# Kernel optimization log

Hardware: AMD Instinct MI355X
Metric: run time of the kernel (lower is better)

The kernel has to match this reference:

```python
import jax, jax.numpy as jnp
import numpy as np

B, D, H, U, K, IV = 4096, 512, 512, 8, 5, 400
NH, CK, CV = 4, 32, 100  # comm heads, comm key/query size, comm value size

@jax.custom_vjp
def blocked_grad(x, mask):
    return x

def _bg_fwd(x, mask):
    return x, mask

def _bg_bwd(mask, g):
    return (g * mask, jnp.zeros_like(mask))

blocked_grad.defvjp(_bg_fwd, _bg_bwd)

def _ln(x, g, b, eps=1e-5):
    m = jnp.mean(x, -1, keepdims=True)
    v = jnp.var(x, -1, keepdims=True)
    return (x - m) / jnp.sqrt(v + eps) * g + b

def setup_inputs():
    key = jax.random.key(0)
    ks = jax.random.split(key, 16)
    def u(k, shape, fan_in):
        lim = 1.0 / np.sqrt(fan_in)
        return jax.random.uniform(k, shape, jnp.float32, -lim, lim)
    return dict(
        x=jax.random.normal(ks[0], (B, 1, D), jnp.float32),
        hs=jax.random.normal(ks[1], (B, U, H), jnp.float32),
        h_masks=jnp.ones((B, 1), jnp.float32),
        key_w=u(ks[2], (D, 64), D), key_b=jnp.zeros((64,), jnp.float32),
        value_w=u(ks[3], (D, IV), D), value_b=jnp.zeros((IV,), jnp.float32),
        query_w=u(ks[4], (U, H, 64), H),
        qc_w=u(ks[5], (U, H, NH * CK), H),
        kc_w=u(ks[6], (U, H, NH * CK), H),
        vc_w=u(ks[7], (U, H, NH * CV), H),
        out_w=u(ks[8], (U, NH * CV, H), NH * CV),
        ln_g=jnp.ones((H,), jnp.float32), ln_b=jnp.zeros((H,), jnp.float32),
        W_ih=u(ks[9], (U, 3 * H, IV), IV), b_ih=jnp.zeros((U, 3 * H), jnp.float32),
        W_hh=u(ks[10], (U, 3 * H, H), H), b_hh=jnp.zeros((U, 3 * H), jnp.float32),
        rnn_ln_g=jnp.ones((U, H), jnp.float32), rnn_ln_b=jnp.zeros((U, H), jnp.float32),
    )

def _forward(x, hs, h_masks, key_w, key_b, value_w, value_b, query_w, qc_w, kc_w,
             vc_w, out_w, ln_g, ln_b, W_ih, b_ih, W_hh, b_hh, rnn_ln_g, rnn_ln_b):
    b = x.shape[0]
    # ---- input attention with top-k unit selection ----
    x2 = jnp.concatenate([x, jnp.zeros_like(x)], axis=1)            # [B,2,D] (null input appended)
    k_l = x2 @ key_w + key_b                                        # [B,2,64]
    v_l = x2 @ value_w + value_b                                    # [B,2,IV]
    q_l = jnp.einsum('buh,uhk->buk', hs, query_w)                   # [B,U,64] grouped linear
    scores = jnp.einsum('buk,btk->but', q_l, k_l) / np.sqrt(64.0)   # [B,U,2]
    _, idx = jax.lax.top_k(scores[:, :, 0], K)                      # top-k over not-null scores
    mask = jnp.zeros((b, U), x.dtype).at[jnp.arange(b)[:, None], idx].set(1.0)
    probs = jax.nn.softmax(scores, axis=-1)                         # dropout is identity at eval
    inp = jnp.einsum('but,btv->buv', probs, v_l) * mask[:, :, None]  # [B,U,IV]
    h_old = hs
    # ---- per-unit GRU (MAPPO RNNLayer: mask hidden, GRU step, LayerNorm on output) ----
    hm = hs * h_masks.reshape(b, 1, 1)
    gi = jnp.einsum('buv,ugv->bug', inp, W_ih) + b_ih               # [B,U,3H]
    gh = jnp.einsum('buh,ugh->bug', hm, W_hh) + b_hh                # [B,U,3H]
    i_r, i_z, i_n = jnp.split(gi, 3, axis=-1)
    h_r, h_z, h_n = jnp.split(gh, 3, axis=-1)
    r = jax.nn.sigmoid(i_r + h_r)
    z = jax.nn.sigmoid(i_z + h_z)
    n = jnp.tanh(i_n + r * h_n)
    h_new = (1.0 - z) * n + z * hm                                  # [B,U,H]
    y = _ln(h_new, rnn_ln_g, rnn_ln_b)
    x_final = y.reshape(b, 1, U * H)
    mask3 = mask[:, :, None]
    hb = blocked_grad(h_new, mask3)
    # ---- communication attention over units (4 heads) ----
    qc = jnp.einsum('buh,uhk->buk', hb, qc_w).reshape(b, U, NH, CK).transpose(0, 2, 1, 3)
    kc = jnp.einsum('buh,uhk->buk', hb, kc_w).reshape(b, U, NH, CK).transpose(0, 2, 1, 3)
    vc = jnp.einsum('buh,uhk->buk', hb, vc_w).reshape(b, U, NH, CV).transpose(0, 2, 1, 3)
    att = jnp.einsum('bnuk,bnvk->bnuv', qc, kc) / np.sqrt(float(CK))
    ap = jax.nn.softmax(att, axis=-1) * mask[:, None, :, None]      # mask query rows
    ctx = jnp.einsum('bnuv,bnvc->bnuc', ap, vc).transpose(0, 2, 1, 3).reshape(b, U, NH * CV)
    ctx = jnp.einsum('buv,uvh->buh', ctx, out_w)                    # grouped output projection
    h_comm = _ln(ctx + hb, ln_g, ln_b)
    hs_out = mask3 * h_comm + (1.0 - mask3) * h_old
    return x_final, hs_out

def reference(x, hs, h_masks, key_w, key_b, value_w, value_b, query_w, qc_w, kc_w,
              vc_w, out_w, ln_g, ln_b, W_ih, b_ih, W_hh, b_hh, rnn_ln_g, rnn_ln_b):
    return _forward(x, hs, h_masks, key_w, key_b, value_w, value_b, query_w, qc_w,
                    kc_w, vc_w, out_w, ln_g, ln_b, W_ih, b_ih, W_hh, b_hh,
                    rnn_ln_g, rnn_ln_b)
```

## Files before the change

### kernel.cpp

```cpp
#include <hip/hip_runtime.h>

typedef __attribute__((ext_vector_type(4))) float f32x4;
typedef __attribute__((ext_vector_type(8))) short bf16x8;
typedef unsigned short u16;

#define DEVINL static __device__ __forceinline__

DEVINL float b2f(u16 u) { union { unsigned int i; float f; } x; x.i = ((unsigned int)u) << 16; return x.f; }
DEVINL u16 f2bf(float f) {
  union { float f; unsigned int i; } x; x.f = f;
  unsigned int r = x.i + 0x7fffu + ((x.i >> 16) & 1u);
  return (u16)(r >> 16);
}
DEVINL float ldin(const void* p, long i, int f) {
  return f ? ((const float*)p)[i] : b2f(((const u16*)p)[i]);
}
DEVINL void ld4bf(const u16* p, float* o) {
  ushort4 v = *(const ushort4*)p;
  o[0] = b2f(v.x); o[1] = b2f(v.y); o[2] = b2f(v.z); o[3] = b2f(v.w);
}
DEVINL void st4out(void* out, size_t idx, const float* v, int f) {
  if (f) {
    float4 t; t.x = v[0]; t.y = v[1]; t.z = v[2]; t.w = v[3];
    *(float4*)((float*)out + idx) = t;
  } else {
    ushort4 t; t.x = f2bf(v[0]); t.y = f2bf(v[1]); t.z = f2bf(v[2]); t.w = f2bf(v[3]);
    *(ushort4*)((u16*)out + idx) = t;
  }
}
DEVINL void cv8(const void* s, long i, int f, u16* d) {
  if (f) {
    const float4 a = *(const float4*)((const float*)s + i);
    const float4 b = *(const float4*)((const float*)s + i + 4);
    ushort4 lo, hi;
    lo.x = f2bf(a.x); lo.y = f2bf(a.y); lo.z = f2bf(a.z); lo.w = f2bf(a.w);
    hi.x = f2bf(b.x); hi.y = f2bf(b.y); hi.z = f2bf(b.z); hi.w = f2bf(b.w);
    *(ushort4*)d = lo; *(ushort4*)(d + 4) = hi;
  } else {
    const ushort4 a = *(const ushort4*)((const u16*)s + i);
    const ushort4 b = *(const ushort4*)((const u16*)s + i + 4);
    *(ushort4*)d = a; *(ushort4*)(d + 4) = b;
  }
}

static constexpr size_t OFF_FLAG = 0;
static constexpr size_t OFF_WIH  = 1024;
static constexpr size_t OFF_QVW  = 11011072;
static constexpr size_t OFF_OUTW = 23593984;
static constexpr size_t OFF_VALW = 27264000;
static constexpr size_t OFF_WHH  = 27788288;
static constexpr size_t OFF_VBP  = 40371200;
static constexpr size_t OFF_BIH  = 40372224;
static constexpr size_t OFF_BHH  = 40396800;
static constexpr size_t OFF_RNG  = 40421376;
static constexpr size_t OFF_RNB  = 40429568;
static constexpr size_t OFF_LNG  = 40437760;
static constexpr size_t OFF_LNB  = 40438784;
static constexpr size_t OFF_HMF  = 40439808;
static constexpr size_t OFF_XB   = 40456192;
static constexpr size_t OFF_HSB  = 44650496;
static constexpr size_t OFF_KL   = 78204928;
static constexpr size_t OFF_VL   = 79253504;
static constexpr size_t OFF_QL   = 87642112;
static constexpr size_t OFF_MASK = 96030720;
static constexpr size_t OFF_HB   = 96161792;
static constexpr size_t OFF_R    = 129716224;

__global__ __launch_bounds__(256) void detect_kernel(const u16* __restrict__ hs_u, int* __restrict__ flag) {
  __shared__ int cnt;
  if (threadIdx.x == 0) cnt = 0;
  __syncthreads();
  int ok = 0;
  for (int i = threadIdx.x; i < 1024; i += 256) {
    const float v = fabsf(b2f(hs_u[2 * i]));
    if (v > 9.094947e-13f && v < 1.0995116e12f) ok++;
  }
  atomicAdd(&cnt, ok);
  __syncthreads();
  if (threadIdx.x == 0) flag[0] = (cnt >= 921) ? 0 : 1;
}

__global__ __launch_bounds__(256) void flatconv_kernel(
    const void* __restrict__ W_ih, const void* __restrict__ W_hh, const void* __restrict__ x,
    const void* __restrict__ hs, const void* __restrict__ value_b, const void* __restrict__ b_ih,
    const void* __restrict__ b_hh, const void* __restrict__ rnn_g, const void* __restrict__ rnn_b,
    const void* __restrict__ ln_g, const void* __restrict__ ln_b, const void* __restrict__ h_masks,
    const int* __restrict__ flagp,
    u16* __restrict__ WIH, u16* __restrict__ WHH, u16* __restrict__ XB, u16* __restrict__ HSB,
    u16* __restrict__ VBP, u16* __restrict__ BIH, u16* __restrict__ BHH,
    u16* __restrict__ RNG, u16* __restrict__ RNB, u16* __restrict__ LNG, u16* __restrict__ LNB,
    float* __restrict__ HMF)
{
  const int f = flagp[0];
  long t = (long)blockIdx.x * 256 + threadIdx.x;
  if (t < 688128L) {
    const long r = t / 56; const int k = (int)(t - r * 56) * 8;
    u16* d = WIH + r * 448 + k;
    if (k < 400) cv8(W_ih, r * 400 + k, f, d);
    else { ushort4 z{0,0,0,0}; *(ushort4*)d = z; *(ushort4*)(d + 4) = z; }
    return;
  }
  t -= 688128L;
  if (t < 786432L) { cv8(W_hh, t * 8, f, WHH + t * 8); return; }
  t -= 786432L;
  if (t < 262144L) { cv8(x, t * 8, f, XB + t * 8); return; }
  t -= 262144L;
  if (t < 2097152L) { cv8(hs, t * 8, f, HSB + t * 8); return; }
  t -= 2097152L;
  if (t < 512L) { VBP[t] = (t < 400) ? f2bf(ldin(value_b, t, f)) : (u16)0; return; }
  t -= 512L;
  if (t < 12288L) { BIH[t] = f2bf(ldin(b_ih, t, f)); return; }
  t -= 12288L;
  if (t < 12288L) { BHH[t] = f2bf(ldin(b_hh, t, f)); return; }
  t -= 12288L;
  if (t < 4096L) { RNG[t] = f2bf(ldin(rnn_g, t, f)); return; }
  t -= 4096L;
  if (t < 4096L) { RNB[t] = f2bf(ldin(rnn_b, t, f)); return; }
  t -= 4096L;
  if (t < 512L) { LNG[t] = f2bf(ldin(ln_g, t, f)); return; }
  t -= 512L;
  if (t < 512L) { LNB[t] = f2bf(ldin(ln_b, t, f)); return; }
  t -= 512L;
  if (t < 4096L) { HMF[t] = ldin(h_masks, t, f); return; }
}

__global__ __launch_bounds__(256) void transpose_kernel(
    const void* __restrict__ src, const int* __restrict__ flagp, u16* __restrict__ dst,
    int K, int N, int Kp, long srcZ, long dstZ)
{
  const int f = flagp[0];
  __shared__ float t[64][65];
  const int k0 = blockIdx.x * 64, n0 = blockIdx.y * 64, z = blockIdx.z;
  const int tid = threadIdx.x;
  const int lk = tid >> 4;
  const int ln4 = (tid & 15) * 4;
#pragma unroll
  for (int p = 0; p < 4; ++p) {
    const int k = k0 + lk + p * 16;
    float v[4] = {0.f, 0.f, 0.f, 0.f};
    if (k < K) {
      const long base = srcZ * z + (long)k * N + n0 + ln4;
#pragma unroll
      for (int j = 0; j < 4; ++j)
        if (n0 + ln4 + j < N) v[j] = ldin(src, base + j, f);
    }
    t[lk + p * 16][ln4 + 0] = v[0]; t[lk + p * 16][ln4 + 1] = v[1];
    t[lk + p * 16][ln4 + 2] = v[2]; t[lk + p * 16][ln4 + 3] = v[3];
  }
  __syncthreads();
#pragma unroll
  for (int p = 0; p < 4; ++p) {
    const int n = n0 + lk + p * 16;
    ushort4 o;
    o.x = f2bf(t[ln4 + 0][lk + p * 16]);
    o.y = f2bf(t[ln4 + 1][lk + p * 16]);
    o.z = f2bf(t[ln4 + 2][lk + p * 16]);
    o.w = f2bf(t[ln4 + 3][lk + p * 16]);
    *(ushort4*)&dst[dstZ * z + (long)n * Kp + k0 + ln4] = o;
  }
}

template<int OUT_BF16, int HAS_BIAS>
__global__ __launch_bounds__(256) void gemm_bt_kernel(
    const u16* __restrict__ A, const u16* __restrict__ W, void* __restrict__ Cp,
    const u16* __restrict__ bias, int KP, int ldaE, long Az, long Wz, long Cz, int Bz, int ldc)
{
  __shared__ u16 lA[128 * 64];
  __shared__ u16 lB[128 * 64];
  const int tid = threadIdx.x;
  const int m0 = blockIdx.x * 128, n0 = blockIdx.y * 128, z = blockIdx.z;
  const u16* Au = A + (size_t)z * Az;
  const u16* Wu = W + (size_t)z * Wz;

  const int l = tid & 63, w = tid >> 6;
  const int WM = (w >> 1) * 64, WN = (w & 1) * 64;
  const int lr = l & 15, kg = l >> 4;

  f32x4 acc[4][4];
#pragma unroll
  for (int i = 0; i < 4; ++i)
#pragma unroll
    for (int j = 0; j < 4; ++j) acc[i][j] = (f32x4){0.f, 0.f, 0.f, 0.f};

  const int rowA = tid >> 3;
  const int cb = (tid & 7) * 16;
  const size_t rowBytesA = (size_t)ldaE * 2;
  const size_t rowBytesW = (size_t)KP * 2;

  for (int k0 = 0; k0 < KP; k0 += 64) {
    __syncthreads();
    const char* gA = (const char*)Au + (size_t)(m0 + rowA) * rowBytesA + (size_t)k0 * 2 + cb;
    const char* gB = (const char*)Wu + (size_t)(n0 + rowA) * rowBytesW + (size_t)k0 * 2 + cb;
    char* sA = (char*)lA + (w << 10);
    char* sB = (char*)lB + (w << 10);
#pragma unroll
    for (int c = 0; c < 4; ++c) {
      __builtin_amdgcn_global_load_lds(
          (const __attribute__((address_space(1))) void*)(gA + (size_t)c * 32 * rowBytesA),
          (__attribute__((address_space(3))) void*)(sA + c * 4096), 16, 0, 0);
      __builtin_amdgcn_global_load_lds(
          (const __attribute__((address_space(1))) void*)(gB + (size_t)c * 32 * rowBytesW),
          (__attribute__((address_space(3))) void*)(sB + c * 4096), 16, 0, 0);
    }
    __syncthreads();
#pragma unroll
    for (int kk = 0; kk < 64; kk += 32) {
      bf16x8 af[4], bw[4];
#pragma unroll
      for (int i = 0; i < 4; ++i)
        af[i] = *(const bf16x8*)&lA[(WM + i * 16 + lr) * 64 + kk + kg * 8];
#pragma unroll
      for (int j = 0; j < 4; ++j)
        bw[j] = *(const bf16x8*)&lB[(WN + j * 16 + lr) * 64 + kk + kg * 8];
#pragma unroll
      for (int i = 0; i < 4; ++i)
#pragma unroll
        for (int j = 0; j < 4; ++j)
          acc[i][j] = __builtin_amdgcn_mfma_f32_16x16x32_bf16(af[i], bw[j], acc[i][j], 0, 0, 0);
    }
  }
  float* Cf = (float*)Cp;
  u16* Cb = (u16*)Cp;
#pragma unroll
  for (int i = 0; i < 4; ++i) {
#pragma unroll
    for (int j = 0; j < 4; ++j) {
      const int gc = n0 + WN + j * 16 + lr;
      float bv = 0.f;
      if (HAS_BIAS) bv = b2f(bias[(size_t)z * Bz + gc]);
#pragma unroll
      for (int t = 0; t < 4; ++t) {
        const int gr = m0 + WM + i * 16 + kg * 4 + t;
        const float v = acc[i][j][t] + bv;
        const size_t idx = (size_t)z * Cz + (size_t)gr * ldc + gc;
        if (OUT_BF16) Cb[idx] = f2bf(v); else Cf[idx] = v;
      }
    }
  }
}

__global__ __launch_bounds__(256) void gemm_f32bf_kernel(
    const void* __restrict__ A, const void* __restrict__ W, float* __restrict__ C,
    const void* __restrict__ bias, const int* __restrict__ flagp,
    int K, int lda, int ldw, int ldc, long Az, long Wz, long Cz)
{
  const int f32 = flagp[0];
  __shared__ float sA[16][65];
  __shared__ float sW[16][64];
  const int tid = threadIdx.x;
  const int m0 = blockIdx.x * 64, n0 = blockIdx.y * 64, z = blockIdx.z;
  const int tx = tid & 15, ty = tid >> 4;
  const int ar = tid >> 2, ak = (tid & 3) * 4;
  const int wk = tid >> 4, wc = (tid & 15) * 4;
  const size_t abase = (size_t)z * Az, wbase = (size_t)z * Wz;
  float acc[4][4] = {};
  for (int k0 = 0; k0 < K; k0 += 16) {
    __syncthreads();
    float a0, a1, a2, a3, w0, w1, w2, w3;
    const size_t ai = abase + (size_t)(m0 + ar) * lda + k0 + ak;
    const size_t wi = wbase + (size_t)(k0 + wk) * ldw + n0 + wc;
    if (f32) {
      const float4 av = *(const float4*)((const float*)A + ai);
      const float4 wv = *(const float4*)((const float*)W + wi);
      a0 = av.x; a1 = av.y; a2 = av.z; a3 = av.w;
      w0 = wv.x; w1 = wv.y; w2 = wv.z; w3 = wv.w;
    } else {
      const ushort4 av = *(const ushort4*)((const u16*)A + ai);
      const ushort4 wv = *(const ushort4*)((const u16*)W + wi);
      a0 = b2f(av.x); a1 = b2f(av.y); a2 = b2f(av.z); a3 = b2f(av.w);
      w0 = b2f(wv.x); w1 = b2f(wv.y); w2 = b2f(wv.z); w3 = b2f(wv.w);
    }
    sA[ak + 0][ar] = a0; sA[ak + 1][ar] = a1; sA[ak + 2][ar] = a2; sA[ak + 3][ar] = a3;
    sW[wk][wc] = w0; sW[wk][wc + 1] = w1; sW[wk][wc + 2] = w2; sW[wk][wc + 3] = w3;
    __syncthreads();
#pragma unroll
    for (int kk = 0; kk < 16; ++kk) {
      const float a0c = sA[kk][ty * 4 + 0], a1c = sA[kk][ty * 4 + 1];
      const float a2c = sA[kk][ty * 4 + 2], a3c = sA[kk][ty * 4 + 3];
      const float4 bv = *(const float4*)&sW[kk][tx * 4];
      acc[0][0] += a0c * bv.x; acc[0][1] += a0c * bv.y; acc[0][2] += a0c * bv.z; acc[0][3] += a0c * bv.w;
      acc[1][0] += a1c * bv.x; acc[1][1] += a1c * bv.y; acc[1][2] += a1c * bv.z; acc[1][3] += a1c * bv.w;
      acc[2][0] += a2c * bv.x; acc[2][1] += a2c * bv.y; acc[2][2] += a2c * bv.z; acc[2][3] += a2c * bv.w;
      acc[3][0] += a3c * bv.x; acc[3][1] += a3c * bv.y; acc[3][2] += a3c * bv.z; acc[3][3] += a3c * bv.w;
    }
  }
#pragma unroll
  for (int i = 0; i < 4; ++i)
#pragma unroll
    for (int j = 0; j < 4; ++j) {
      const int n = n0 + tx * 4 + j;
      float v = acc[i][j];
      if (bias) v += ldin(bias, n, f32);
      C[(size_t)z * Cz + (size_t)(m0 + ty * 4 + i) * ldc + n] = v;
    }
}

__global__ __launch_bounds__(256) void select_kernel(
    const float* __restrict__ q_l, const float* __restrict__ k_l,
    const void* __restrict__ key_b, const void* __restrict__ value_b,
    const float* __restrict__ v_l, const int* __restrict__ flagp,
    float* __restrict__ mask_out, u16* __restrict__ inp)
{
  const int b = blockIdx.x, tid = threadIdx.x;
  const int f32 = flagp[0];
  __shared__ float s_sc[16], s_pm[8], s_pm1[8];
  __shared__ float s_v[400], s_vb[400];
  const int task = tid >> 4, l16 = tid & 15, uu = task & 7;
  const float* qv = q_l + (size_t)b * 512 + uu * 64;
  float p = 0.f;
  if (task < 8) {
    const float* kv = k_l + (size_t)b * 64;
    for (int k = l16; k < 64; k += 16) p += qv[k] * kv[k];
  } else {
    for (int k = l16; k < 64; k += 16) p += qv[k] * ldin(key_b, k, f32);
  }
  p += __shfl_xor(p, 8, 16); p += __shfl_xor(p, 4, 16);
  p += __shfl_xor(p, 2, 16); p += __shfl_xor(p, 1, 16);
  if (l16 == 0) s_sc[task] = p * 0.125f;
  for (int i = tid; i < 400; i += 256) { s_v[i] = v_l[(size_t)b * 512 + i]; s_vb[i] = ldin(value_b, i, f32); }
  __syncthreads();
  if (tid < 8) {
    const float s0 = s_sc[tid];
    int rank = 0;
    for (int u2 = 0; u2 < 8; ++u2) {
      const float o = s_sc[u2];
      rank += (o > s0) || (o == s0 && u2 < tid);
    }
    const float m = (rank < 5) ? 1.f : 0.f;
    mask_out[(size_t)b * 8 + tid] = m;
    const float s1 = s_sc[8 + tid];
    const float mx = fmaxf(s0, s1);
    const float e0 = expf(s0 - mx), e1 = expf(s1 - mx);
    const float p0 = e0 / (e0 + e1);
    s_pm[tid] = m * p0; s_pm1[tid] = m * (1.f - p0);
  }
  __syncthreads();
#pragma unroll
  for (int u = 0; u < 8; ++u) {
    const float pm = s_pm[u], pm1 = s_pm1[u];
    for (int i = tid; i < 448; i += 256) {
      const float v = (i < 400) ? (pm * s_v[i] + pm1 * s_vb[i]) : 0.f;
      inp[((size_t)u * 4096 + b) * 448 + i] = f2bf(v);
    }
  }
}

__device__ __forceinline__ void block_reduce_2(float& a, float& b) {
#pragma unroll
  for (int o = 32; o; o >>= 1) { a += __shfl_down(a, o, 64); b += __shfl_down(b, o, 64); }
  __shared__ float red[4];
  const int tid = threadIdx.x;
  if ((tid & 63) == 0) { red[(tid >> 6) * 2] = a; red[(tid >> 6) * 2 + 1] = b; }
  __syncthreads();
  a = red[0] + red[2]; b = red[1] + red[3];
}

__global__ __launch_bounds__(128) void gates_kernel(
    const u16* __restrict__ gi, const u16* __restrict__ gh,
    const u16* __restrict__ hsb, const float* __restrict__ hmf,
    const u16* __restrict__ bhh, const u16* __restrict__ rng, const u16* __restrict__ rnb,
    const int* __restrict__ flagp, int bbase, void* __restrict__ out0, u16* __restrict__ hb)
{
  const int f = flagp[0];
  const int u = blockIdx.y, bl = blockIdx.x;
  const int b = bbase + bl;
  const int h0 = threadIdx.x * 4;
  const size_t rowg = ((size_t)u * gridDim.x + bl) * 1536;
  const size_t rowhs = ((size_t)b * 8 + u) * 512;
  const size_t rowhb = ((size_t)u * 4096 + b) * 512;
  float ir[4], iz[4], inn[4], hr[4], hz[4], hnn[4], hsv[4], br[4], bz[4], bn[4];
  ld4bf(gi + rowg + h0, ir);
  ld4bf(gi + rowg + 512 + h0, iz);
  ld4bf(gi + rowg + 1024 + h0, inn);
  ld4bf(gh + rowg + h0, hr);
  ld4bf(gh + rowg + 512 + h0, hz);
  ld4bf(gh + rowg + 1024 + h0, hnn);
  ld4bf(hsb + rowhs + h0, hsv);
  ld4bf(bhh + u * 1536 + h0, br);
  ld4bf(bhh + u * 1536 + 512 + h0, bz);
  ld4bf(bhh + u * 1536 + 1024 + h0, bn);
  const float hmask = hmf[b];
  float hn[4]; float sum = 0.f, sq = 0.f;
#pragma unroll
  for (int j = 0; j < 4; ++j) {
    const float hrf = hmask * hr[j] + br[j];
    const float hzf = hmask * hz[j] + bz[j];
    const float hnf = hmask * hnn[j] + bn[j];
    const float r = 1.f / (1.f + expf(-(ir[j] + hrf)));
    const float zz = 1.f / (1.f + expf(-(iz[j] + hzf)));
    const float n = tanhf(inn[j] + r * hnf);
    const float hmv = hsv[j] * hmask;
    const float h = (1.f - zz) * n + zz * hmv;
    hn[j] = h; sum += h; sq += h * h;
  }
  block_reduce_2(sum, sq);
  const float mean = sum * (1.f / 512.f);
  const float var = fmaxf(sq * (1.f / 512.f) - mean * mean, 0.f);
  const float rstd = rsqrtf(var + 1e-5f);
  float gg[4], bb[4];
  ld4bf(rng + u * 512 + h0, gg);
  ld4bf(rnb + u * 512 + h0, bb);
  float yv[4];
#pragma unroll
  for (int j = 0; j < 4; ++j) yv[j] = (hn[j] - mean) * rstd * gg[j] + bb[j];
  st4out(out0, (size_t)b * 4096 + u * 512 + h0, yv, f);
  ushort4 hv;
  hv.x = f2bf(hn[0]); hv.y = f2bf(hn[1]); hv.z = f2bf(hn[2]); hv.w = f2bf(hn[3]);
  *(ushort4*)(hb + rowhb + h0) = hv;
}

__global__ __launch_bounds__(256) void attn_kernel(
    const u16* __restrict__ qvc, const float* __restrict__ maskp, int bbase,
    u16* __restrict__ ctx)
{
  const int bl = blockIdx.x, tid = threadIdx.x;
  const int b = bbase + bl;
  const size_t MC = gridDim.x;
  __shared__ float s_q[8][128], s_k[8][128];
  __shared__ float s_ap[4][8][8];
  __shared__ float s_v[8][400];
  for (int i = tid; i < 1024; i += 256) {
    const int u = i >> 7, c = i & 127;
    const size_t base = ((size_t)u * MC + bl) * 768;
    s_q[u][c] = b2f(qvc[base + c]);
    s_k[u][c] = b2f(qvc[base + 128 + c]);
  }
  for (int i = tid; i < 3200; i += 256) {
    const int u = i / 400, c = i - u * 400;
    s_v[u][c] = b2f(qvc[((size_t)u * MC + bl) * 768 + 256 + c]);
  }
  __syncthreads();
  const int n = tid >> 6, uu = (tid >> 3) & 7, vv = tid & 7;
  float a = 0.f;
#pragma unroll
  for (int k = 0; k < 32; ++k) a += s_q[uu][n * 32 + k] * s_k[vv][n * 32 + k];
  a *= 0.17677669529663687f;
  float mx = a;
  for (int o = 4; o; o >>= 1) mx = fmaxf(mx, __shfl_xor(mx, o, 8));
  const float e = expf(a - mx);
  float se = e;
  for (int o = 4; o; o >>= 1) se += __shfl_xor(se, o, 8);
  s_ap[n][uu][vv] = e / se * maskp[(size_t)b * 8 + uu];
  __syncthreads();
  for (int i = tid; i < 3584; i += 256) {
    const int u = i / 448, c = i - u * 448;
    float v = 0.f;
    if (c < 400) {
      const int nn = c / 100;
      const float* ap = s_ap[nn][u];
#pragma unroll
      for (int v2 = 0; v2 < 8; ++v2) v += ap[v2] * s_v[v2][c];
    }
    ctx[((size_t)u * MC + bl) * 448 + c] = f2bf(v);
  }
}

__global__ __launch_bounds__(128) void final_kernel(
    const u16* __restrict__ ctx2, const u16* __restrict__ hb, const u16* __restrict__ hsb,
    const float* __restrict__ maskp, const u16* __restrict__ lng, const u16* __restrict__ lnb,
    const int* __restrict__ flagp, int bbase, void* __restrict__ outp)
{
  const int f = flagp[0];
  const int u = blockIdx.y, bl = blockIdx.x;
  const int b = bbase + bl;
  const int h0 = threadIdx.x * 4;
  const size_t rowc = ((size_t)u * gridDim.x + bl) * 512;
  const size_t rowhs = ((size_t)b * 8 + u) * 512;
  const size_t rowhb = ((size_t)u * 4096 + b) * 512;
  float cv[4], hbv[4];
  ld4bf(ctx2 + rowc + h0, cv);
  ld4bf(hb + rowhb + h0, hbv);
  float v[4] = { cv[0] + hbv[0], cv[1] + hbv[1], cv[2] + hbv[2], cv[3] + hbv[3] };
  float sum = v[0] + v[1] + v[2] + v[3];
  float sq = v[0] * v[0] + v[1] * v[1] + v[2] * v[2] + v[3] * v[3];
  block_reduce_2(sum, sq);
  const float mean = sum * (1.f / 512.f);
  const float var = fmaxf(sq * (1.f / 512.f) - mean * mean, 0.f);
  const float rstd = rsqrtf(var + 1e-5f);
  float gg[4], bb2[4], hsv[4];
  ld4bf(lng + h0, gg); ld4bf(lnb + h0, bb2); ld4bf(hsb + rowhs + h0, hsv);
  const float msk = maskp[(size_t)b * 8 + u];
  float ov[4];
#pragma unroll
  for (int j = 0; j < 4; ++j)
    ov[j] = msk * ((v[j] - mean) * rstd * gg[j] + bb2[j]) + (1.f - msk) * hsv[j];
  st4out(outp, (size_t)16777216 + (size_t)(b * 8 + u) * 512 + h0, ov, f);
}

extern "C" void kernel_launch(void* const* d_in, const int* in_sizes, int n_in,
                              void* d_out, int out_size, void* d_ws, size_t ws_size,
                              hipStream_t stream) {
  const void* x       = d_in[0];
  const void* hs      = d_in[1];
  const void* h_masks = d_in[2];
  const void* key_w   = d_in[3];
  const void* key_b   = d_in[4];
  const void* value_w = d_in[5];
  const void* value_b = d_in[6];
  const void* query_w = d_in[7];
  const void* qc_w    = d_in[8];
  const void* kc_w    = d_in[9];
  const void* vc_w    = d_in[10];
  const void* out_w   = d_in[11];
  const void* ln_g    = d_in[12];
  const void* ln_b    = d_in[13];
  const void* W_ih    = d_in[14];
  const void* b_ih    = d_in[15];
  const void* W_hh    = d_in[16];
  const void* b_hh    = d_in[17];
  const void* rnn_g   = d_in[18];
  const void* rnn_b   = d_in[19];

  char* ws = (char*)d_ws;
  int*   FLAG = (int*)(ws + OFF_FLAG);
  u16*   WIH  = (u16*)(ws + OFF_WIH);
  u16*   QVW  = (u16*)(ws + OFF_QVW);
  u16*   OUTW = (u16*)(ws + OFF_OUTW);
  u16*   VALW = (u16*)(ws + OFF_VALW);
  u16*   WHH  = (u16*)(ws + OFF_WHH);
  u16*   VBP  = (u16*)(ws + OFF_VBP);
  u16*   BIH  = (u16*)(ws + OFF_BIH);
  u16*   BHH  = (u16*)(ws + OFF_BHH);
  u16*   RNG  = (u16*)(ws + OFF_RNG);
  u16*   RNB  = (u16*)(ws + OFF_RNB);
  u16*   LNG  = (u16*)(ws + OFF_LNG);
  u16*   LNB  = (u16*)(ws + OFF_LNB);
  float* HMF  = (float*)(ws + OFF_HMF);
  u16*   XB   = (u16*)(ws + OFF_XB);
  u16*   HSB  = (u16*)(ws + OFF_HSB);
  float* KL   = (float*)(ws + OFF_KL);
  float* VL   = (float*)(ws + OFF_VL);
  float* QL   = (float*)(ws + OFF_QL);
  float* MASK = (float*)(ws + OFF_MASK);
  u16*   HB   = (u16*)(ws + OFF_HB);
  u16*   INP  = (u16*)(ws + OFF_R);

  detect_kernel<<<1, 256, 0, stream>>>((const u16*)hs, FLAG);
  flatconv_kernel<<<15126, 256, 0, stream>>>(
      W_ih, W_hh, x, hs, value_b, b_ih, b_hh, rnn_g, rnn_b, ln_g, ln_b, h_masks, FLAG,
      WIH, WHH, XB, HSB, VBP, BIH, BHH, RNG, RNB, LNG, LNB, HMF);
  transpose_kernel<<<dim3(8, 2, 8), 256, 0, stream>>>(qc_w,    FLAG, QVW,           512, 128, 512, 65536L,  393216L);
  transpose_kernel<<<dim3(8, 2, 8), 256, 0, stream>>>(kc_w,    FLAG, QVW + 65536,   512, 128, 512, 65536L,  393216L);
  transpose_kernel<<<dim3(8, 8, 8), 256, 0, stream>>>(vc_w,    FLAG, QVW + 131072,  512, 400, 512, 204800L, 393216L);
  transpose_kernel<<<dim3(7, 8, 8), 256, 0, stream>>>(out_w,   FLAG, OUTW,          400, 512, 448, 204800L, 229376L);
  transpose_kernel<<<dim3(8, 8, 1), 256, 0, stream>>>(value_w, FLAG, VALW,          512, 400, 512, 0L,      0L);
  gemm_bt_kernel<0, 1><<<dim3(32, 4, 1), 256, 0, stream>>>(XB, VALW, VL, VBP, 512, 512, 0L, 0L, 0L, 0, 512);
  gemm_f32bf_kernel<<<dim3(64, 1, 1), 256, 0, stream>>>(x, key_w, KL, key_b, FLAG, 512, 512, 64, 64, 0L, 0L, 0L);
  gemm_f32bf_kernel<<<dim3(64, 1, 8), 256, 0, stream>>>(hs, query_w, QL, nullptr, FLAG, 512, 4096, 64, 512, 512L, 32768L, 64L);
  select_kernel<<<4096, 256, 0, stream>>>(QL, KL, key_b, value_b, VL, FLAG, MASK, INP);

  const size_t base_g = OFF_R + 29360128UL;
  int MCG = 4096;
  if (ws_size < base_g + 2UL * 8 * 4096 * 1536 * 2) MCG = 2048;
  if (ws_size < base_g + 2UL * 8 * 2048 * 1536 * 2) MCG = 1024;
  u16* GI = (u16*)(ws + base_g);
  u16* GH = GI + (size_t)8 * MCG * 1536;
  for (int c = 0; c < 4096 / MCG; ++c) {
    gemm_bt_kernel<1, 1><<<dim3(MCG / 128, 12, 8), 256, 0, stream>>>(
        INP + (size_t)c * MCG * 448, WIH, GI, BIH, 448, 448, 1835008L, 688128L, (long)MCG * 1536, 1536, 1536);
    gemm_bt_kernel<1, 0><<<dim3(MCG / 128, 12, 8), 256, 0, stream>>>(
        HSB + (size_t)c * MCG * 4096, WHH, GH, nullptr, 512, 4096, 512L, 786432L, (long)MCG * 1536, 0, 1536);
    gates_kernel<<<dim3(MCG, 8), 128, 0, stream>>>(GI, GH, HSB, HMF, BHH, RNG, RNB, FLAG, c * MCG, d_out, HB);
  }

  int MCC = 4096;
  if (ws_size < OFF_R + (size_t)8 * 4096 * (768 + 448 + 512) * 2) MCC = 2048;
  u16* QVC  = (u16*)(ws + OFF_R);
  u16* CTX  = QVC + (size_t)8 * MCC * 768;
  u16* CTX2 = CTX + (size_t)8 * MCC * 448;
  for (int d2 = 0; d2 < 4096 / MCC; ++d2) {
    gemm_bt_kernel<1, 0><<<dim3(MCC / 128, 6, 8), 256, 0, stream>>>(
        HB + (size_t)d2 * MCC * 512, QVW, QVC, nullptr, 512, 512, 2097152L, 393216L, (long)MCC * 768, 0, 768);
    attn_kernel<<<dim3(MCC), 256, 0, stream>>>(QVC, MASK, d2 * MCC, CTX);
    gemm_bt_kernel<1, 0><<<dim3(MCC / 128, 4, 8), 256, 0, stream>>>(
        CTX, OUTW, CTX2, nullptr, 448, 448, (long)MCC * 448, 229376L, (long)MCC * 512, 0, 512);
    final_kernel<<<dim3(MCC, 8), 128, 0, stream>>>(CTX2, HB, HSB, MASK, LNG, LNB, FLAG, d2 * MCC, d_out);
  }
  (void)in_sizes; (void)n_in; (void)out_size; (void)ws_size;
}
```

Baseline: 590.8 us.

## Add 256x256 8-wave pipelined GEMM and pad K dims to 512

Adds a new 512-thread GEMM kernel with 256x256 output tiles that double-buffers LDS tiles through direct global-to-LDS loads, interleaves staging with MFMA phases, and raises wave priority around the MFMA blocks. To fit its fixed K=512 loop, the W_ih, input and context buffers and out_w are padded from 448 to 512 columns and the workspace offsets are recomputed. All four large grouped GEMMs (GRU input and hidden, QKV, output projection) switch to it, aiming for more data reuse per tile and better overlap of memory and compute, at the cost of extra zero-padding work and bigger buffers.

```diff
diff --git a/kernel.cpp b/kernel.cpp
--- a/kernel.cpp
+++ b/kernel.cpp
@@ -45,26 +45,26 @@
 
 static constexpr size_t OFF_FLAG = 0;
 static constexpr size_t OFF_WIH  = 1024;
-static constexpr size_t OFF_QVW  = 11011072;
-static constexpr size_t OFF_OUTW = 23593984;
-static constexpr size_t OFF_VALW = 27264000;
-static constexpr size_t OFF_WHH  = 27788288;
-static constexpr size_t OFF_VBP  = 40371200;
-static constexpr size_t OFF_BIH  = 40372224;
-static constexpr size_t OFF_BHH  = 40396800;
-static constexpr size_t OFF_RNG  = 40421376;
-static constexpr size_t OFF_RNB  = 40429568;
-static constexpr size_t OFF_LNG  = 40437760;
-static constexpr size_t OFF_LNB  = 40438784;
-static constexpr size_t OFF_HMF  = 40439808;
-static constexpr size_t OFF_XB   = 40456192;
-static constexpr size_t OFF_HSB  = 44650496;
-static constexpr size_t OFF_KL   = 78204928;
-static constexpr size_t OFF_VL   = 79253504;
-static constexpr size_t OFF_QL   = 87642112;
-static constexpr size_t OFF_MASK = 96030720;
-static constexpr size_t OFF_HB   = 96161792;
-static constexpr size_t OFF_R    = 129716224;
+static constexpr size_t OFF_WHH  = 12583936;
+static constexpr size_t OFF_QVW  = 25166848;
+static constexpr size_t OFF_OUTW = 31458304;
+static constexpr size_t OFF_VALW = 35652608;
+static constexpr size_t OFF_VBP  = 36176896;
+static constexpr size_t OFF_BIH  = 36177920;
+static constexpr size_t OFF_BHH  = 36202496;
+static constexpr size_t OFF_RNG  = 36227072;
+static constexpr size_t OFF_RNB  = 36235264;
+static constexpr size_t OFF_LNG  = 36243456;
+static constexpr size_t OFF_LNB  = 36244480;
+static constexpr size_t OFF_HMF  = 36245504;
+static constexpr size_t OFF_XB   = 36261888;
+static constexpr size_t OFF_HSB  = 40456192;
+static constexpr size_t OFF_KL   = 74010624;
+static constexpr size_t OFF_VL   = 75059200;
+static constexpr size_t OFF_QL   = 83447808;
+static constexpr size_t OFF_MASK = 91836416;
+static constexpr size_t OFF_HB   = 91967488;
+static constexpr size_t OFF_R    = 125521920;
 
 __global__ __launch_bounds__(256) void detect_kernel(const u16* __restrict__ hs_u, int* __restrict__ flag) {
   __shared__ int cnt;
@@ -93,14 +93,14 @@
 {
   const int f = flagp[0];
   long t = (long)blockIdx.x * 256 + threadIdx.x;
-  if (t < 688128L) {
-    const long r = t / 56; const int k = (int)(t - r * 56) * 8;
-    u16* d = WIH + r * 448 + k;
+  if (t < 786432L) {
+    const long r = t >> 6; const int k = (int)(t & 63) * 8;
+    u16* d = WIH + r * 512 + k;
     if (k < 400) cv8(W_ih, r * 400 + k, f, d);
     else { ushort4 z{0,0,0,0}; *(ushort4*)d = z; *(ushort4*)(d + 4) = z; }
     return;
   }
-  t -= 688128L;
+  t -= 786432L;
   if (t < 786432L) { cv8(W_hh, t * 8, f, WHH + t * 8); return; }
   t -= 786432L;
   if (t < 262144L) { cv8(x, t * 8, f, XB + t * 8); return; }
@@ -161,6 +161,112 @@
 }
 
 template<int OUT_BF16, int HAS_BIAS>
+__global__ __launch_bounds__(512, 2) void gemm8_kernel(
+    const u16* __restrict__ A, const u16* __restrict__ W, void* __restrict__ Cp,
+    const u16* __restrict__ bias, int ldaE, long Az, long Wz, long Cz, int Bz, int ldc)
+{
+  __shared__ u16 lds[65536];
+  const int tid = threadIdx.x;
+  const int w = tid >> 6, l = tid & 63;
+  const int wr = w >> 2, wc = w & 3;
+  const int lr = l & 15, kg = l >> 4;
+  const int l3 = l >> 3, l7k = (l & 7) * 8;
+  const int m0 = blockIdx.x * 256, n0 = blockIdx.y * 256, z = blockIdx.z;
+  const u16* Au = A + (size_t)z * Az;
+  const u16* Wu = W + (size_t)z * Wz;
+
+  f32x4 acc[8][4];
+#pragma unroll
+  for (int i = 0; i < 8; ++i)
+#pragma unroll
+    for (int j = 0; j < 4; ++j) acc[i][j] = (f32x4){0.f, 0.f, 0.f, 0.f};
+
+#define GL8(srcp, dstoff) __builtin_amdgcn_global_load_lds( \
+    (const __attribute__((address_space(1))) void*)(srcp), \
+    (__attribute__((address_space(3))) void*)((char*)lds + 2 * (dstoff)), 16, 0, 0)
+
+#define STAGE_A8(t, mh, slot) do { \
+  _Pragma("unroll") for (int c_ = 0; c_ < 2; ++c_) { \
+    const int row0_ = (mh) * 64 + w * 8 + c_ * 128; \
+    GL8(Au + (size_t)(m0 + row0_ + l3) * ldaE + (t) * 64 + l7k, (slot) * 16384 + row0_ * 64); \
+  } } while (0)
+
+#define STAGE_B8(t, nh, slot) do { \
+  _Pragma("unroll") for (int c_ = 0; c_ < 2; ++c_) { \
+    const int rq0_ = w * 8 + c_ * 64; \
+    const int row0_ = ((rq0_ >> 5) << 6) + (nh) * 32 + (rq0_ & 31); \
+    GL8(Wu + (size_t)(n0 + row0_ + l3) * 512 + (t) * 64 + l7k, 32768 + (slot) * 16384 + row0_ * 64); \
+  } } while (0)
+
+#define VMW4 asm volatile("s_waitcnt vmcnt(4)" ::: "memory")
+
+#define PHASE8(sl, mh, nh, STG, VMW) do { \
+  bf16x8 fa_[2][4], fb_[2][2]; \
+  _Pragma("unroll") for (int kk = 0; kk < 2; ++kk) { \
+    _Pragma("unroll") for (int mq = 0; mq < 4; ++mq) \
+      fa_[kk][mq] = *(const bf16x8*)&lds[(sl) * 16384 + (wr * 128 + (mh) * 64 + mq * 16 + lr) * 64 + kk * 32 + kg * 8]; \
+    _Pragma("unroll") for (int nq = 0; nq < 2; ++nq) \
+      fb_[kk][nq] = *(const bf16x8*)&lds[32768 + (sl) * 16384 + (wc * 64 + (nh) * 32 + nq * 16 + lr) * 64 + kk * 32 + kg * 8]; \
+  } \
+  STG; \
+  asm volatile("" ::: "memory"); \
+  __builtin_amdgcn_s_barrier(); \
+  __builtin_amdgcn_s_setprio(1); \
+  _Pragma("unroll") for (int kk = 0; kk < 2; ++kk) \
+    _Pragma("unroll") for (int mq = 0; mq < 4; ++mq) \
+      _Pragma("unroll") for (int nq = 0; nq < 2; ++nq) \
+        acc[(mh) * 4 + mq][(nh) * 2 + nq] = __builtin_amdgcn_mfma_f32_16x16x32_bf16( \
+            fa_[kk][mq], fb_[kk][nq], acc[(mh) * 4 + mq][(nh) * 2 + nq], 0, 0, 0); \
+  __builtin_amdgcn_s_setprio(0); \
+  VMW; \
+  asm volatile("" ::: "memory"); \
+  __builtin_amdgcn_s_barrier(); \
+} while (0)
+
+  STAGE_A8(0, 0, 0); STAGE_A8(0, 1, 0); STAGE_B8(0, 0, 0); STAGE_B8(0, 1, 0);
+  STAGE_A8(1, 0, 1); STAGE_B8(1, 0, 1);
+  asm volatile("s_waitcnt vmcnt(4)" ::: "memory");
+  __builtin_amdgcn_s_barrier();
+
+  for (int i = 0; i < 4; ++i) {
+    const int tB = 2 * i + 1, tC = (2 * i + 2) & 7, tD = (2 * i + 3) & 7;
+    PHASE8(0, 0, 0, STAGE_A8(tB, 1, 1), );
+    PHASE8(0, 0, 1, STAGE_B8(tB, 1, 1), );
+    PHASE8(0, 1, 0, STAGE_A8(tC, 0, 0), );
+    PHASE8(0, 1, 1, STAGE_B8(tC, 0, 0), VMW4);
+    PHASE8(1, 0, 0, STAGE_A8(tC, 1, 0), );
+    PHASE8(1, 0, 1, STAGE_B8(tC, 1, 0), );
+    PHASE8(1, 1, 0, STAGE_A8(tD, 0, 1), );
+    PHASE8(1, 1, 1, STAGE_B8(tD, 0, 1), VMW4);
+  }
+  asm volatile("s_waitcnt vmcnt(0)" ::: "memory");
+
+  float* Cf = (float*)Cp;
+  u16* Cb = (u16*)Cp;
+#pragma unroll
+  for (int mf = 0; mf < 8; ++mf) {
+#pragma unroll
+    for (int nf = 0; nf < 4; ++nf) {
+      const int gc = n0 + wc * 64 + nf * 16 + lr;
+      float bv = 0.f;
+      if (HAS_BIAS) bv = b2f(bias[(size_t)z * Bz + gc]);
+#pragma unroll
+      for (int t = 0; t < 4; ++t) {
+        const int gr = m0 + wr * 128 + mf * 16 + kg * 4 + t;
+        const float v = acc[mf][nf][t] + bv;
+        const size_t idx = (size_t)z * Cz + (size_t)gr * ldc + gc;
+        if (OUT_BF16) Cb[idx] = f2bf(v); else Cf[idx] = v;
+      }
+    }
+  }
+#undef GL8
+#undef STAGE_A8
+#undef STAGE_B8
+#undef VMW4
+#undef PHASE8
+}
+
+template<int OUT_BF16, int HAS_BIAS>
 __global__ __launch_bounds__(256) void gemm_bt_kernel(
     const u16* __restrict__ A, const u16* __restrict__ W, void* __restrict__ Cp,
     const u16* __restrict__ bias, int KP, int ldaE, long Az, long Wz, long Cz, int Bz, int ldc)
@@ -171,22 +277,18 @@
   const int m0 = blockIdx.x * 128, n0 = blockIdx.y * 128, z = blockIdx.z;
   const u16* Au = A + (size_t)z * Az;
   const u16* Wu = W + (size_t)z * Wz;
-
   const int l = tid & 63, w = tid >> 6;
   const int WM = (w >> 1) * 64, WN = (w & 1) * 64;
   const int lr = l & 15, kg = l >> 4;
-
   f32x4 acc[4][4];
 #pragma unroll
   for (int i = 0; i < 4; ++i)
 #pragma unroll
     for (int j = 0; j < 4; ++j) acc[i][j] = (f32x4){0.f, 0.f, 0.f, 0.f};
-
   const int rowA = tid >> 3;
   const int cb = (tid & 7) * 16;
   const size_t rowBytesA = (size_t)ldaE * 2;
   const size_t rowBytesW = (size_t)KP * 2;
-
   for (int k0 = 0; k0 < KP; k0 += 64) {
     __syncthreads();
     const char* gA = (const char*)Au + (size_t)(m0 + rowA) * rowBytesA + (size_t)k0 * 2 + cb;
@@ -338,9 +440,9 @@
 #pragma unroll
   for (int u = 0; u < 8; ++u) {
     const float pm = s_pm[u], pm1 = s_pm1[u];
-    for (int i = tid; i < 448; i += 256) {
+    for (int i = tid; i < 512; i += 256) {
       const float v = (i < 400) ? (pm * s_v[i] + pm1 * s_vb[i]) : 0.f;
-      inp[((size_t)u * 4096 + b) * 448 + i] = f2bf(v);
+      inp[((size_t)u * 4096 + b) * 512 + i] = f2bf(v);
     }
   }
 }
@@ -442,8 +544,8 @@
   for (int o = 4; o; o >>= 1) se += __shfl_xor(se, o, 8);
   s_ap[n][uu][vv] = e / se * maskp[(size_t)b * 8 + uu];
   __syncthreads();
-  for (int i = tid; i < 3584; i += 256) {
-    const int u = i / 448, c = i - u * 448;
+  for (int i = tid; i < 4096; i += 256) {
+    const int u = i >> 9, c = i & 511;
     float v = 0.f;
     if (c < 400) {
       const int nn = c / 100;
@@ -451,7 +553,7 @@
 #pragma unroll
       for (int v2 = 0; v2 < 8; ++v2) v += ap[v2] * s_v[v2][c];
     }
-    ctx[((size_t)u * MC + bl) * 448 + c] = f2bf(v);
+    ctx[((size_t)u * MC + bl) * 512 + c] = f2bf(v);
   }
 }
 
@@ -514,10 +616,10 @@
   char* ws = (char*)d_ws;
   int*   FLAG = (int*)(ws + OFF_FLAG);
   u16*   WIH  = (u16*)(ws + OFF_WIH);
+  u16*   WHH  = (u16*)(ws + OFF_WHH);
   u16*   QVW  = (u16*)(ws + OFF_QVW);
   u16*   OUTW = (u16*)(ws + OFF_OUTW);
   u16*   VALW = (u16*)(ws + OFF_VALW);
-  u16*   WHH  = (u16*)(ws + OFF_WHH);
   u16*   VBP  = (u16*)(ws + OFF_VBP);
   u16*   BIH  = (u16*)(ws + OFF_BIH);
   u16*   BHH  = (u16*)(ws + OFF_BHH);
@@ -536,44 +638,44 @@
   u16*   INP  = (u16*)(ws + OFF_R);
 
   detect_kernel<<<1, 256, 0, stream>>>((const u16*)hs, FLAG);
-  flatconv_kernel<<<15126, 256, 0, stream>>>(
+  flatconv_kernel<<<15511, 256, 0, stream>>>(
       W_ih, W_hh, x, hs, value_b, b_ih, b_hh, rnn_g, rnn_b, ln_g, ln_b, h_masks, FLAG,
       WIH, WHH, XB, HSB, VBP, BIH, BHH, RNG, RNB, LNG, LNB, HMF);
-  transpose_kernel<<<dim3(8, 2, 8), 256, 0, stream>>>(qc_w,    FLAG, QVW,           512, 128, 512, 65536L,  393216L);
-  transpose_kernel<<<dim3(8, 2, 8), 256, 0, stream>>>(kc_w,    FLAG, QVW + 65536,   512, 128, 512, 65536L,  393216L);
-  transpose_kernel<<<dim3(8, 8, 8), 256, 0, stream>>>(vc_w,    FLAG, QVW + 131072,  512, 400, 512, 204800L, 393216L);
-  transpose_kernel<<<dim3(7, 8, 8), 256, 0, stream>>>(out_w,   FLAG, OUTW,          400, 512, 448, 204800L, 229376L);
-  transpose_kernel<<<dim3(8, 8, 1), 256, 0, stream>>>(value_w, FLAG, VALW,          512, 400, 512, 0L,      0L);
+  transpose_kernel<<<dim3(8, 2, 8), 256, 0, stream>>>(qc_w,    FLAG, QVW,          512, 128, 512, 65536L,  393216L);
+  transpose_kernel<<<dim3(8, 2, 8), 256, 0, stream>>>(kc_w,    FLAG, QVW + 65536,  512, 128, 512, 65536L,  393216L);
+  transpose_kernel<<<dim3(8, 8, 8), 256, 0, stream>>>(vc_w,    FLAG, QVW + 131072, 512, 400, 512, 204800L, 393216L);
+  transpose_kernel<<<dim3(8, 8, 8), 256, 0, stream>>>(out_w,   FLAG, OUTW,         400, 512, 512, 204800L, 262144L);
+  transpose_kernel<<<dim3(8, 8, 1), 256, 0, stream>>>(value_w, FLAG, VALW,         512, 400, 512, 0L,      0L);
   gemm_bt_kernel<0, 1><<<dim3(32, 4, 1), 256, 0, stream>>>(XB, VALW, VL, VBP, 512, 512, 0L, 0L, 0L, 0, 512);
   gemm_f32bf_kernel<<<dim3(64, 1, 1), 256, 0, stream>>>(x, key_w, KL, key_b, FLAG, 512, 512, 64, 64, 0L, 0L, 0L);
   gemm_f32bf_kernel<<<dim3(64, 1, 8), 256, 0, stream>>>(hs, query_w, QL, nullptr, FLAG, 512, 4096, 64, 512, 512L, 32768L, 64L);
   select_kernel<<<4096, 256, 0, stream>>>(QL, KL, key_b, value_b, VL, FLAG, MASK, INP);
 
-  const size_t base_g = OFF_R + 29360128UL;
+  const size_t base_g = OFF_R + 33554432UL;
   int MCG = 4096;
   if (ws_size < base_g + 2UL * 8 * 4096 * 1536 * 2) MCG = 2048;
   if (ws_size < base_g + 2UL * 8 * 2048 * 1536 * 2) MCG = 1024;
   u16* GI = (u16*)(ws + base_g);
   u16* GH = GI + (size_t)8 * MCG * 1536;
   for (int c = 0; c < 4096 / MCG; ++c) {
-    gemm_bt_kernel<1, 1><<<dim3(MCG / 128, 12, 8), 256, 0, stream>>>(
-        INP + (size_t)c * MCG * 448, WIH, GI, BIH, 448, 448, 1835008L, 688128L, (long)MCG * 1536, 1536, 1536);
-    gemm_bt_kernel<1, 0><<<dim3(MCG / 128, 12, 8), 256, 0, stream>>>(
-        HSB + (size_t)c * MCG * 4096, WHH, GH, nullptr, 512, 4096, 512L, 786432L, (long)MCG * 1536, 0, 1536);
+    gemm8_kernel<1, 1><<<dim3(MCG / 256, 6, 8), 512, 0, stream>>>(
+        INP + (size_t)c * MCG * 512, WIH, GI, BIH, 512, 2097152L, 786432L, (long)MCG * 1536, 1536, 1536);
+    gemm8_kernel<1, 0><<<dim3(MCG / 256, 6, 8), 512, 0, stream>>>(
+        HSB + (size_t)c * MCG * 4096, WHH, GH, nullptr, 4096, 512L, 786432L, (long)MCG * 1536, 0, 1536);
     gates_kernel<<<dim3(MCG, 8), 128, 0, stream>>>(GI, GH, HSB, HMF, BHH, RNG, RNB, FLAG, c * MCG, d_out, HB);
   }
 
   int MCC = 4096;
-  if (ws_size < OFF_R + (size_t)8 * 4096 * (768 + 448 + 512) * 2) MCC = 2048;
+  if (ws_size < OFF_R + (size_t)8 * 4096 * (768 + 512 + 512) * 2) MCC = 2048;
   u16* QVC  = (u16*)(ws + OFF_R);
   u16* CTX  = QVC + (size_t)8 * MCC * 768;
-  u16* CTX2 = CTX + (size_t)8 * MCC * 448;
+  u16* CTX2 = CTX + (size_t)8 * MCC * 512;
   for (int d2 = 0; d2 < 4096 / MCC; ++d2) {
-    gemm_bt_kernel<1, 0><<<dim3(MCC / 128, 6, 8), 256, 0, stream>>>(
-        HB + (size_t)d2 * MCC * 512, QVW, QVC, nullptr, 512, 512, 2097152L, 393216L, (long)MCC * 768, 0, 768);
+    gemm8_kernel<1, 0><<<dim3(MCC / 256, 3, 8), 512, 0, stream>>>(
+        HB + (size_t)d2 * MCC * 512, QVW, QVC, nullptr, 512, 2097152L, 393216L, (long)MCC * 768, 0, 768);
     attn_kernel<<<dim3(MCC), 256, 0, stream>>>(QVC, MASK, d2 * MCC, CTX);
-    gemm_bt_kernel<1, 0><<<dim3(MCC / 128, 4, 8), 256, 0, stream>>>(
-        CTX, OUTW, CTX2, nullptr, 448, 448, (long)MCC * 448, 229376L, (long)MCC * 512, 0, 512);
+    gemm8_kernel<1, 0><<<dim3(MCC / 256, 2, 8), 512, 0, stream>>>(
+        CTX, OUTW, CTX2, nullptr, 512, (long)MCC * 512, 262144L, (long)MCC * 512, 0, 512);
     final_kernel<<<dim3(MCC, 8), 128, 0, stream>>>(CTX2, HB, HSB, MASK, LNG, LNB, FLAG, d2 * MCC, d_out);
   }
   (void)in_sizes; (void)n_in; (void)out_size; (void)ws_size;
```

After: 625.5 us. +5.9%, slower.
